# Kernel tuning notes

Hardware: AMD Instinct MI355X
Metric: run time of the kernel (lower is better)

Reference implementation:

```python
import jax, jax.numpy as jnp
import numpy as np

B, N, K = 8, 2048, 20
IN_CHAN = 3
CONV_DIMS = (64, 64, 128, 256)
FEAT_DIM = 1024
SLOPE = 0.2  # LeakyReLU negative slope (DGCNN standard)


def setup_inputs() -> dict:
    key = jax.random.key(0)
    ks = jax.random.split(key, 11)
    x = jax.random.normal(ks[0], (B, N, IN_CHAN), dtype=jnp.float32)
    in_dims = (IN_CHAN,) + CONV_DIMS[:-1]
    inp = {"x": x}
    for i, (cin, cout) in enumerate(zip(in_dims, CONV_DIMS)):
        inp[f"W{i+1}"] = jax.random.normal(ks[1 + 2 * i], (cout, 2 * cin), dtype=jnp.float32) * 0.05
        inp[f"b{i+1}"] = jnp.zeros((cout,), dtype=jnp.float32)
    inp["Wf"] = jax.random.normal(ks[9], (FEAT_DIM, sum(CONV_DIMS)), dtype=jnp.float32) * 0.05
    inp["bf"] = jnp.zeros((FEAT_DIM,), dtype=jnp.float32)
    return inp


def _knn_idx(x, k):
    # x: (B, N, C) -> indices of k nearest neighbors (self included), (B, N, K)
    xx = jnp.sum(x * x, axis=-1)                       # (B, N)
    inner = jnp.einsum('bnc,bmc->bnm', x, x)           # (B, N, N)
    d2 = xx[:, :, None] - 2.0 * inner + xx[:, None, :]  # squared distances
    _, idx = jax.lax.top_k(-d2, k)                     # k smallest distances
    return idx


def _edge_conv(x, W, b, k):
    # x: (B, N, C); W: (O, 2C); b: (O,) -> (B, N, O)
    idx = _knn_idx(x, k)                               # (B, N, K)
    nbr = jax.vmap(lambda xb, ib: xb[ib])(x, idx)      # (B, N, K, C) gather
    center = jnp.broadcast_to(x[:, :, None, :], nbr.shape)
    feat = jnp.concatenate([nbr - center, center], axis=-1)  # (B, N, K, 2C)
    h = jnp.einsum('bnkc,oc->bnko', feat, W) + b       # 1x1 conv over edges
    h = jax.nn.leaky_relu(h, SLOPE)
    return jnp.max(h, axis=2)                          # max over neighbors


def reference(x, W1, b1, W2, b2, W3, b3, W4, b4, Wf, bf):
    params = [(W1, b1), (W2, b2), (W3, b3), (W4, b4)]
    feats = []
    h = x
    for W, b in params:
        h = _edge_conv(h, W, b, K)
        feats.append(h)
    hcat = jnp.concatenate(feats, axis=-1)             # (B, N, sum(conv_dims))
    out = jnp.einsum('bnc,oc->bno', hcat, Wf) + bf     # final 1x1 conv
    out = jax.nn.leaky_relu(out, SLOPE)
    return jnp.max(out, axis=1)                        # global max pool -> (B, FEAT_DIM)
```

## Files before the change

kernel.cpp:

```cpp
#include <hip/hip_runtime.h>

constexpr int B_ = 8;
constexpr int N_ = 2048;
constexpr int K_ = 20;
constexpr float SLOPE_ = 0.2f;

typedef __attribute__((ext_vector_type(8))) short bf16x8;
typedef __attribute__((ext_vector_type(8))) _Float16 f16x8;
typedef __attribute__((ext_vector_type(4))) float f32x4;

__device__ __forceinline__ float lrelu(float v) { return v > 0.0f ? v : SLOPE_ * v; }

__device__ __forceinline__ void async16(const void* g, void* l) {
  __builtin_amdgcn_global_load_lds((const __attribute__((address_space(1))) unsigned int*)g,
                                   (__attribute__((address_space(3))) unsigned int*)l, 16, 0, 0);
}

__device__ __forceinline__ unsigned long long shflx64(unsigned long long v, int m) {
  return __shfl_xor(v, m, 64);
}

__device__ __forceinline__ unsigned short f2bf(float f) {
  unsigned u = __float_as_uint(f);
  u += 0x7fff + ((u >> 16) & 1);
  return (unsigned short)(u >> 16);
}

__device__ __forceinline__ unsigned short f2h(float f) {
  _Float16 h = (_Float16)f;
  return __builtin_bit_cast(unsigned short, h);
}
__device__ __forceinline__ float h2f(unsigned short u) {
  return (float)__builtin_bit_cast(_Float16, u);
}

__global__ void prep_wp(const float* __restrict__ W, float* __restrict__ Wp,
                        unsigned short* __restrict__ Wp_bf, int O, int C) {
  int i = blockIdx.x * 256 + threadIdx.x;
  if (i >= 2 * O * C) return;
  int o = i / C, c = i - o * C;
  float v;
  if (o < O)
    v = W[o * 2 * C + c];
  else
    v = W[(o - O) * 2 * C + C + c] - W[(o - O) * 2 * C + c];
  Wp[i] = v;
  if (Wp_bf) Wp_bf[i] = f2bf(v);
}

__global__ void cvt_bf16(const float4* __restrict__ src, ushort4* __restrict__ dst, int n4) {
  int i = blockIdx.x * 256 + threadIdx.x;
  if (i >= n4) return;
  float4 v = src[i];
  ushort4 o = {f2bf(v.x), f2bf(v.y), f2bf(v.z), f2bf(v.w)};
  dst[i] = o;
}

__global__ void split32_x(const float* __restrict__ x, unsigned short* __restrict__ xh,
                          unsigned short* __restrict__ xm, float* __restrict__ xx) {
  int id = blockIdx.x * 256 + threadIdx.x;
  if (id >= B_ * N_ * 32) return;
  int row = id >> 5, c = id & 31;
  float val = (c < 3) ? x[row * 3 + c] : 0.0f;
  unsigned short hb = f2h(val);
  float vh = h2f(hb);
  xh[id] = hb;
  xm[id] = f2h(val - vh);
  float sq = val * val;
#pragma unroll
  for (int off = 16; off > 0; off >>= 1) sq += __shfl_xor(sq, off, 32);
  if (c == 0) xx[row] = sq;
}

template <int C>
__global__ void pack_knn(const unsigned short* __restrict__ Xh,
                         const unsigned short* __restrict__ Xm,
                         unsigned short* __restrict__ Pk) {
  constexpr int KK = C / 32;
  int id = blockIdx.x * 256 + threadIdx.x;
  const int outoff = id;
  const int l = id & 63;
  id >>= 6;
  const int split = id & 1;
  id >>= 1;
  const int kk = id % KK;
  id /= KK;
  const int tile = id & 127;
  const int b = id >> 7;
  const unsigned short* src = (split == 0) ? Xh : Xm;
  const size_t soff =
      (size_t)(b * N_ + tile * 16 + (l & 15)) * C + (size_t)kk * 32 + (size_t)(l >> 4) * 8;
  uint4 v = *(const uint4*)(src + soff);
  *(uint4*)(Pk + (size_t)outoff * 8) = v;
}

__device__ __forceinline__ void select_topk(const float* __restrict__ d2row, int lane,
                                            unsigned long long* __restrict__ cb,
                                            int* __restrict__ outp) {
  float r2[32];
#pragma unroll
  for (int i = 0; i < 32; i++) r2[i] = d2row[i * 64 + lane];

  const float INF = __int_as_float(0x7f800000);

  float lmin = r2[0];
#pragma unroll
  for (int i = 1; i < 32; i++) lmin = fminf(lmin, r2[i]);
  float sv = lmin;
#pragma unroll
  for (int k = 2; k <= 64; k <<= 1)
#pragma unroll
    for (int j = k >> 1; j > 0; j >>= 1) {
      float p = __shfl_xor(sv, j, 64);
      bool takeMax = ((lane & j) != 0) == ((lane & k) == 0);
      sv = takeMax ? fmaxf(sv, p) : fminf(sv, p);
    }
  float T = __shfl(sv, 19, 64);

  unsigned cnt = 0;
#pragma unroll
  for (int i = 0; i < 32; i++) {
    bool pred = r2[i] <= T;
    unsigned long long mk = __ballot(pred);
    if (mk) {
      int off = __popcll(mk & ((1ull << lane) - 1ull));
      unsigned pos = cnt + (unsigned)off;
      if (pred && pos < 64)
        cb[pos] = ((unsigned long long)__float_as_uint(r2[i]) << 32) | (unsigned)(i * 64 + lane);
      cnt += (unsigned)__popcll(mk);
    }
  }

  if (cnt <= 64) {
    unsigned long long v = (lane < (int)cnt) ? cb[lane] : ~0ull;
#pragma unroll
    for (int k = 2; k <= 64; k <<= 1)
#pragma unroll
      for (int j = k >> 1; j > 0; j >>= 1) {
        unsigned long long p = shflx64(v, j);
        bool takeMax = ((lane & j) != 0) == ((lane & k) == 0);
        bool lt = v < p;
        v = (takeMax == lt) ? p : v;
      }
    if (lane < K_) outp[lane] = (int)(unsigned)(v & 0xffffffffull);
  } else {
    for (int t2 = 0; t2 < K_; t2++) {
      unsigned long long loc = ~0ull;
#pragma unroll
      for (int i = 0; i < 32; i++) {
        unsigned long long u =
            ((unsigned long long)__float_as_uint(r2[i]) << 32) | (unsigned)(i * 64 + lane);
        loc = u < loc ? u : loc;
      }
#pragma unroll
      for (int off = 32; off > 0; off >>= 1) {
        unsigned long long vv = shflx64(loc, off);
        loc = vv < loc ? vv : loc;
      }
      const int mwin = (int)(unsigned)(loc & 0xffffffffull);
      if (lane == 0) outp[t2] = mwin;
#pragma unroll
      for (int i = 0; i < 32; i++)
        if (i * 64 + lane == mwin) r2[i] = INF;
    }
  }
}

template <int C>
__global__ __launch_bounds__(1024, 4) void knn_mfma_q16(const unsigned short* __restrict__ Pk,
                                                        const unsigned short* __restrict__ Xh,
                                                        const unsigned short* __restrict__ Xm,
                                                        const float* __restrict__ xx,
                                                        int* __restrict__ idxo) {
  constexpr int KK = C / 32;
  constexpr int DP = 3;
  constexpr int NIT = KK * 8;
  const int b = blockIdx.x & 7;
  const int q0 = (blockIdx.x >> 3) * 16;
  const int tid = threadIdx.x;
  const int w = tid >> 6, lane = tid & 63;
  const int bN = b * N_;
  const int lr = lane & 15;
  const int lk = (lane >> 4) * 8;

  __shared__ float d2s[16][2052];
  __shared__ unsigned long long cbuf[16][64];

  const size_t qoff = (size_t)(bN + q0 + lr) * C + lk;
  f16x8 a2h[2], a2m[2];
  a2h[0] = *(const f16x8*)(Xh + qoff);
  a2m[0] = *(const f16x8*)(Xm + qoff);

  f32x4 acc[8];
#pragma unroll
  for (int t = 0; t < 8; t++) acc[t] = (f32x4){0.0f, 0.0f, 0.0f, 0.0f};

  const size_t pbase = (size_t)b * (128 * KK * 2 * 512) + (size_t)lane * 8;
  f16x8 bh[DP], bm[DP];
#pragma unroll
  for (int i = 0; i < DP; i++) {
    const size_t a = pbase + (size_t)(((w * 8 + i) * KK + 0) * 2) * 512;
    bh[i] = *(const f16x8*)(Pk + a);
    bm[i] = *(const f16x8*)(Pk + a + 512);
  }
#pragma unroll
  for (int it = 0; it < NIT; it++) {
    const int kk = it >> 3, t = it & 7, s = it % DP;
    if (t == 0 && kk + 1 < KK) {
      const size_t qa = qoff + (size_t)(kk + 1) * 32;
      a2h[(kk + 1) & 1] = *(const f16x8*)(Xh + qa);
      a2m[(kk + 1) & 1] = *(const f16x8*)(Xm + qa);
    }
    f16x8 vh = bh[s], vm = bm[s];
    if (it + DP < NIT) {
      const int it2 = it + DP;
      const int kk2 = it2 >> 3, t2 = it2 & 7;
      const size_t a = pbase + (size_t)(((w * 8 + t2) * KK + kk2) * 2) * 512;
      bh[s] = *(const f16x8*)(Pk + a);
      bm[s] = *(const f16x8*)(Pk + a + 512);
    }
    const f16x8 ah = a2h[kk & 1], am = a2m[kk & 1];
    acc[t] = __builtin_amdgcn_mfma_f32_16x16x32_f16(ah, vh, acc[t], 0, 0, 0);
    acc[t] = __builtin_amdgcn_mfma_f32_16x16x32_f16(ah, vm, acc[t], 0, 0, 0);
    acc[t] = __builtin_amdgcn_mfma_f32_16x16x32_f16(am, vh, acc[t], 0, 0, 0);
    acc[t] = __builtin_amdgcn_mfma_f32_16x16x32_f16(am, vm, acc[t], 0, 0, 0);
  }

  float qn[4];
#pragma unroll
  for (int r = 0; r < 4; r++) qn[r] = xx[bN + q0 + (lane >> 4) * 4 + r];
#pragma unroll
  for (int t = 0; t < 8; t++) {
    float cn = xx[bN + (w * 8 + t) * 16 + lr];
#pragma unroll
    for (int r = 0; r < 4; r++) {
      float v = fmaxf(fmaf(-2.0f, acc[t][r], cn + qn[r]), 0.0f);
      d2s[(lane >> 4) * 4 + r][(w * 8 + t) * 16 + lr] = v;
    }
  }
  __syncthreads();
  select_topk(&d2s[w][0], lane, cbuf[w], idxo + (size_t)(bN + q0 + w) * K_);
}

template <int C>
__global__ __launch_bounds__(512, 2) void knn_mfma_q32(const unsigned short* __restrict__ Pk,
                                                       const unsigned short* __restrict__ Xh,
                                                       const unsigned short* __restrict__ Xm,
                                                       const float* __restrict__ xx,
                                                       int* __restrict__ idxo) {
  constexpr int KK = C / 32;
  constexpr int NIT = KK * 16;
  const int b = blockIdx.x & 7;
  const int q0 = (blockIdx.x >> 3) * 32;
  const int tid = threadIdx.x;
  const int w = tid >> 6, lane = tid & 63;
  const int bN = b * N_;
  const int lr = lane & 15;
  const int lk = (lane >> 4) * 8;

  __shared__ float d2s[16][2052];
  __shared__ unsigned long long cbuf[8][64];

  const size_t qoff0 = (size_t)(bN + q0 + lr) * C + lk;
  const size_t qoff1 = (size_t)(bN + q0 + 16 + lr) * C + lk;

  f32x4 acc0[16], acc1[16];
#pragma unroll
  for (int t = 0; t < 16; t++) {
    acc0[t] = (f32x4){0.0f, 0.0f, 0.0f, 0.0f};
    acc1[t] = (f32x4){0.0f, 0.0f, 0.0f, 0.0f};
  }

  const size_t pbase = (size_t)b * (128 * KK * 2 * 512) + (size_t)lane * 8;
  f16x8 bh[2], bm[2];
#pragma unroll
  for (int i = 0; i < 2; i++) {
    const size_t a = pbase + (size_t)(((w * 16 + i) * KK + 0) * 2) * 512;
    bh[i] = *(const f16x8*)(Pk + a);
    bm[i] = *(const f16x8*)(Pk + a + 512);
  }
  f16x8 ah0, am0, ah1, am1;
#pragma unroll
  for (int it = 0; it < NIT; it++) {
    const int kk = it >> 4, t = it & 15, s = it & 1;
    if (t == 0) {
      ah0 = *(const f16x8*)(Xh + qoff0 + (size_t)kk * 32);
      am0 = *(const f16x8*)(Xm + qoff0 + (size_t)kk * 32);
      ah1 = *(const f16x8*)(Xh + qoff1 + (size_t)kk * 32);
      am1 = *(const f16x8*)(Xm + qoff1 + (size_t)kk * 32);
    }
    f16x8 vh = bh[s], vm = bm[s];
    if (it + 2 < NIT) {
      const int it2 = it + 2;
      const int kk2 = it2 >> 4, t2 = it2 & 15;
      const size_t a = pbase + (size_t)(((w * 16 + t2) * KK + kk2) * 2) * 512;
      bh[s] = *(const f16x8*)(Pk + a);
      bm[s] = *(const f16x8*)(Pk + a + 512);
    }
    acc0[t] = __builtin_amdgcn_mfma_f32_16x16x32_f16(ah0, vh, acc0[t], 0, 0, 0);
    acc0[t] = __builtin_amdgcn_mfma_f32_16x16x32_f16(ah0, vm, acc0[t], 0, 0, 0);
    acc0[t] = __builtin_amdgcn_mfma_f32_16x16x32_f16(am0, vh, acc0[t], 0, 0, 0);
    acc0[t] = __builtin_amdgcn_mfma_f32_16x16x32_f16(am0, vm, acc0[t], 0, 0, 0);
    acc1[t] = __builtin_amdgcn_mfma_f32_16x16x32_f16(ah1, vh, acc1[t], 0, 0, 0);
    acc1[t] = __builtin_amdgcn_mfma_f32_16x16x32_f16(ah1, vm, acc1[t], 0, 0, 0);
    acc1[t] = __builtin_amdgcn_mfma_f32_16x16x32_f16(am1, vh, acc1[t], 0, 0, 0);
    acc1[t] = __builtin_amdgcn_mfma_f32_16x16x32_f16(am1, vm, acc1[t], 0, 0, 0);
  }

  float qn0[4], qn1[4];
#pragma unroll
  for (int r = 0; r < 4; r++) {
    qn0[r] = xx[bN + q0 + (lane >> 4) * 4 + r];
    qn1[r] = xx[bN + q0 + 16 + (lane >> 4) * 4 + r];
  }

#pragma unroll
  for (int t = 0; t < 16; t++) {
    const int tt = w * 16 + t;
    float cn = xx[bN + tt * 16 + lr];
#pragma unroll
    for (int r = 0; r < 4; r++)
      d2s[(lane >> 4) * 4 + r][tt * 16 + lr] = fmaxf(fmaf(-2.0f, acc0[t][r], cn + qn0[r]), 0.0f);
  }
  __syncthreads();
  select_topk(&d2s[2 * w + 0][0], lane, cbuf[w], idxo + (size_t)(bN + q0 + 2 * w + 0) * K_);
  select_topk(&d2s[2 * w + 1][0], lane, cbuf[w], idxo + (size_t)(bN + q0 + 2 * w + 1) * K_);
  __syncthreads();

#pragma unroll
  for (int t = 0; t < 16; t++) {
    const int tt = w * 16 + t;
    float cn = xx[bN + tt * 16 + lr];
#pragma unroll
    for (int r = 0; r < 4; r++)
      d2s[(lane >> 4) * 4 + r][tt * 16 + lr] = fmaxf(fmaf(-2.0f, acc1[t][r], cn + qn1[r]), 0.0f);
  }
  __syncthreads();
  select_topk(&d2s[2 * w + 0][0], lane, cbuf[w], idxo + (size_t)(bN + q0 + 16 + 2 * w + 0) * K_);
  select_topk(&d2s[2 * w + 1][0], lane, cbuf[w], idxo + (size_t)(bN + q0 + 16 + 2 * w + 1) * K_);
}

template <int C, int O2>
__global__ void proj_kernel(const float* __restrict__ hin, int stride,
                            const float* __restrict__ Wp, float* __restrict__ P) {
  const int nt = (blockIdx.x & 7) * N_ + (blockIdx.x >> 3) * 16;
  const int o = blockIdx.y * blockDim.x + threadIdx.x;
  __shared__ float hs[16][C];
  for (int i = threadIdx.x; i < 16 * C; i += blockDim.x) {
    int r = i / C, c = i - r * C;
    hs[r][c] = hin[(size_t)(nt + r) * stride + c];
  }
  __syncthreads();
  float acc[16];
#pragma unroll
  for (int t = 0; t < 16; t++) acc[t] = 0.0f;
  const float* wr = Wp + (size_t)o * C;
  if constexpr (C % 4 == 0) {
    for (int cg = 0; cg < C; cg += 4) {
      float4 w = *(const float4*)(wr + cg);
#pragma unroll
      for (int t = 0; t < 16; t++) {
        float4 h = *(const float4*)(&hs[t][cg]);
        acc[t] += w.x * h.x + w.y * h.y + w.z * h.z + w.w * h.w;
      }
    }
  } else {
    for (int c = 0; c < C; c++) {
      float w = wr[c];
#pragma unroll
      for (int t = 0; t < 16; t++) acc[t] += w * hs[t][c];
    }
  }
#pragma unroll
  for (int t = 0; t < 16; t++) P[(size_t)(nt + t) * O2 + o] = acc[t];
}

__global__ __launch_bounds__(256) void gemm_proj(const unsigned short* __restrict__ A, int astride,
                                                 const unsigned short* __restrict__ Bw,
                                                 float* __restrict__ P) {
  const int m0 = ((blockIdx.x & 7) * 16 + (blockIdx.x >> 3)) * 128;
  const int n0 = blockIdx.y * 128;
  const int tid = threadIdx.x;
  const int w = tid >> 6, lane = tid & 63;
  const int wm = w & 1, wn = w >> 1;

  __shared__ unsigned short lA[128 * 32];
  __shared__ unsigned short lB[128 * 32];

  const int r0 = (w * 2 + 0) * 16 + (lane >> 2);
  const int r1 = (w * 2 + 1) * 16 + (lane >> 2);
  const int ks = (lane & 3) * 8;
  const unsigned short* a0 = A + (size_t)(m0 + r0) * astride + ks;
  const unsigned short* a1 = A + (size_t)(m0 + r1) * astride + ks;
  const unsigned short* b0 = Bw + (size_t)(n0 + r0) * 128 + ks;
  const unsigned short* b1 = Bw + (size_t)(n0 + r1) * 128 + ks;
  unsigned short* lA0 = lA + (w * 2 + 0) * 512;
  unsigned short* lA1 = lA + (w * 2 + 1) * 512;
  unsigned short* lB0 = lB + (w * 2 + 0) * 512;
  unsigned short* lB1 = lB + (w * 2 + 1) * 512;

  f32x4 acc[4][4] = {};
  const int ka = (lane >> 4) * 8;

  for (int k0 = 0; k0 < 128; k0 += 32) {
    __syncthreads();
    async16(a0 + k0, lA0);
    async16(a1 + k0, lA1);
    async16(b0 + k0, lB0);
    async16(b1 + k0, lB1);
    __syncthreads();
    bf16x8 af[4], bfr[4];
#pragma unroll
    for (int mt = 0; mt < 4; mt++)
      af[mt] = *(const bf16x8*)&lA[(wm * 64 + mt * 16 + (lane & 15)) * 32 + ka];
#pragma unroll
    for (int nt = 0; nt < 4; nt++)
      bfr[nt] = *(const bf16x8*)&lB[(wn * 64 + nt * 16 + (lane & 15)) * 32 + ka];
#pragma unroll
    for (int mt = 0; mt < 4; mt++)
#pragma unroll
      for (int nt = 0; nt < 4; nt++)
        acc[mt][nt] = __builtin_amdgcn_mfma_f32_16x16x32_bf16(af[mt], bfr[nt], acc[mt][nt], 0, 0, 0);
  }

  const int col = n0 + wn * 64 + (lane & 15);
  const int rowb = m0 + wm * 64 + (lane >> 4) * 4;
#pragma unroll
  for (int mt = 0; mt < 4; mt++)
#pragma unroll
    for (int nt = 0; nt < 4; nt++)
#pragma unroll
      for (int r = 0; r < 4; r++)
        P[(size_t)(rowb + mt * 16 + r) * 512 + col + nt * 16] = acc[mt][nt][r];
}

template <int O>
__global__ __launch_bounds__(256) void combine_kernel(
    const float* __restrict__ P, const int* __restrict__ idxo, const float* __restrict__ bias,
    float* __restrict__ hout, unsigned short* __restrict__ hbf, float* __restrict__ xxo,
    unsigned short* __restrict__ xh, unsigned short* __restrict__ xm,
    unsigned short* __restrict__ a4) {
  constexpr int ROWS = 256 / O;
  const int bb = blockIdx.x & 7;
  const int rt = blockIdx.x >> 3;
  const int r = threadIdx.x / O;
  const int o = threadIdx.x & (O - 1);
  const int row = bb * N_ + rt * ROWS + r;
  __shared__ int idxs[ROWS][K_];
  __shared__ float ps[ROWS][O / 64 > 0 ? O / 64 : 1];
  if (o < K_) idxs[r][o] = idxo[(size_t)row * K_ + o];
  __syncthreads();
  const int base_row = bb * N_;
  float g = -3.4e38f;
#pragma unroll
  for (int k = 0; k < K_; k++) {
    float v = P[(size_t)(base_row + idxs[r][k]) * (2 * O) + o];
    g = fmaxf(g, v);
  }
  float ba = P[(size_t)row * (2 * O) + O + o];
  float val = lrelu(g + ba + bias[o]);
  if (hout) hout[(size_t)row * 512 + o] = val;
  if (hbf) hbf[(size_t)row * 512 + o] = f2bf(val);
  if (xh) {
    unsigned short hb = f2h(val);
    float vh = h2f(hb);
    size_t pp = (size_t)row * O + o;
    xh[pp] = hb;
    xm[pp] = f2h(val - vh);
  }
  if (a4) a4[(size_t)row * 1024 + o] = f2bf(val);
  if (xxo) {
    float sq = val * val;
#pragma unroll
    for (int off = 32; off > 0; off >>= 1) sq += __shfl_xor(sq, off, 64);
    if constexpr (O == 64) {
      if (o == 0) xxo[row] = sq;
    } else {
      if ((threadIdx.x & 63) == 0) ps[r][o >> 6] = sq;
      __syncthreads();
      if (o == 0) {
        float t = ps[r][0];
#pragma unroll
        for (int u = 1; u < O / 64; u++) t += ps[r][u];
        xxo[row] = t;
      }
    }
  }
}

__global__ __launch_bounds__(256) void gemm_final(const unsigned short* __restrict__ A,
                                                  const unsigned short* __restrict__ Bw,
                                                  float* __restrict__ part) {
  const int mt5 = (blockIdx.x & 7) * 16 + (blockIdx.x >> 3);
  const int m0 = mt5 * 128;
  const int n0 = blockIdx.y * 128;
  const int tid = threadIdx.x;
  const int w = tid >> 6, lane = tid & 63;
  const int wm = w & 1, wn = w >> 1;

  __shared__ unsigned short lA[128 * 32];
  __shared__ unsigned short lB[128 * 32];
  __shared__ float ldsred[2][128];

  const int r0 = (w * 2 + 0) * 16 + (lane >> 2);
  const int r1 = (w * 2 + 1) * 16 + (lane >> 2);
  const int ks = (lane & 3) * 8;
  const unsigned short* a0 = A + (size_t)(m0 + r0) * 512 + ks;
  const unsigned short* a1 = A + (size_t)(m0 + r1) * 512 + ks;
  const unsigned short* b0 = Bw + (size_t)(n0 + r0) * 512 + ks;
  const unsigned short* b1 = Bw + (size_t)(n0 + r1) * 512 + ks;
  unsigned short* lA0 = lA + (w * 2 + 0) * 512;
  unsigned short* lA1 = lA + (w * 2 + 1) * 512;
  unsigned short* lB0 = lB + (w * 2 + 0) * 512;
  unsigned short* lB1 = lB + (w * 2 + 1) * 512;

  f32x4 acc[4][4] = {};
  const int ka = (lane >> 4) * 8;

  for (int k0 = 0; k0 < 512; k0 += 32) {
    __syncthreads();
    async16(a0 + k0, lA0);
    async16(a1 + k0, lA1);
    async16(b0 + k0, lB0);
    async16(b1 + k0, lB1);
    __syncthreads();
    bf16x8 af[4], bfr[4];
#pragma unroll
    for (int mt = 0; mt < 4; mt++)
      af[mt] = *(const bf16x8*)&lA[(wm * 64 + mt * 16 + (lane & 15)) * 32 + ka];
#pragma unroll
    for (int nt = 0; nt < 4; nt++)
      bfr[nt] = *(const bf16x8*)&lB[(wn * 64 + nt * 16 + (lane & 15)) * 32 + ka];
#pragma unroll
    for (int mt = 0; mt < 4; mt++)
#pragma unroll
      for (int nt = 0; nt < 4; nt++)
        acc[mt][nt] = __builtin_amdgcn_mfma_f32_16x16x32_bf16(af[mt], bfr[nt], acc[mt][nt], 0, 0, 0);
  }

#pragma unroll
  for (int nt = 0; nt < 4; nt++) {
    float v = -3.4e38f;
#pragma unroll
    for (int mt = 0; mt < 4; mt++)
#pragma unroll
      for (int r = 0; r < 4; r++) v = fmaxf(v, acc[mt][nt][r]);
    v = fmaxf(v, __shfl_xor(v, 16, 64));
    v = fmaxf(v, __shfl_xor(v, 32, 64));
    if (lane < 16) ldsred[wm][wn * 64 + nt * 16 + lane] = v;
  }
  __syncthreads();
  if (tid < 128) {
    float v = fmaxf(ldsred[0][tid], ldsred[1][tid]);
    const int b = blockIdx.x & 7, s5 = blockIdx.x >> 3;
    part[(size_t)(b * 16 + s5) * 1024 + n0 + tid] = v;
  }
}

__global__ void final_reduce(const float* __restrict__ part, const float* __restrict__ bf,
                             float* __restrict__ out) {
  int i = blockIdx.x * 256 + threadIdx.x;
  if (i >= B_ * 1024) return;
  int b = i >> 10, o = i & 1023;
  float m = -3.4e38f;
  for (int s = 0; s < 16; s++) m = fmaxf(m, part[(size_t)(b * 16 + s) * 1024 + o]);
  out[i] = lrelu(m + bf[o]);
}

extern "C" void kernel_launch(void* const* d_in, const int* in_sizes, int n_in, void* d_out,
                              int out_size, void* d_ws, size_t ws_size, hipStream_t stream) {
  (void)in_sizes; (void)n_in; (void)out_size;
  const float* x = (const float*)d_in[0];
  const float* W1 = (const float*)d_in[1];
  const float* b1 = (const float*)d_in[2];
  const float* W2 = (const float*)d_in[3];
  const float* b2 = (const float*)d_in[4];
  const float* W3 = (const float*)d_in[5];
  const float* b3 = (const float*)d_in[6];
  const float* W4 = (const float*)d_in[7];
  const float* b4 = (const float*)d_in[8];
  const float* Wf = (const float*)d_in[9];
  const float* bf = (const float*)d_in[10];

  float* ws = (float*)d_ws;
  float* hcat = ws;
  float* P = hcat + (size_t)B_ * N_ * 512;
  int* idx = (int*)(P + (size_t)B_ * N_ * 512);
  float* Wp = (float*)(idx + (size_t)B_ * N_ * K_);
  float* part = Wp + 512 * 128;
  float* xxb = part + 8 * 16 * 1024;
  float* out = (float*)d_out;
  unsigned short* hcat_bf = (unsigned short*)P;
  unsigned short* Wf_bf = hcat_bf + (size_t)B_ * N_ * 512;
  unsigned short* A4_bf = (unsigned short*)hcat + 512;
  unsigned short* Wp_bf = (unsigned short*)part;

  float* ws_end = xxb + (size_t)B_ * N_;
  unsigned short* hcatbf2 = (unsigned short*)ws_end;
  const size_t need = ((char*)(hcatbf2 + (size_t)B_ * N_ * 512)) - (char*)d_ws;
  const bool fused = ws_size >= need;

  unsigned short* Xh23 = (unsigned short*)(P + (size_t)2097152);
  unsigned short* Xm23 = Xh23 + (size_t)B_ * N_ * 64;
  unsigned short* Xh4 = (unsigned short*)(P + (size_t)4194304);
  unsigned short* Xm4 = Xh4 + (size_t)B_ * N_ * 128;
  unsigned short* Xh1 = Xh23;
  unsigned short* Xm1 = Xh1 + (size_t)B_ * N_ * 32;
  unsigned short* Pk = (unsigned short*)P;

  dim3 knng16(N_ / 16 * B_);
  dim3 knng32q(N_ / 32 * B_);
  const int pk_blocks32 = B_ * 128 * 1 * 2 * 64 / 256;
  const int pk_blocks64 = B_ * 128 * 2 * 2 * 64 / 256;
  const int pk_blocks128 = B_ * 128 * 4 * 2 * 64 / 256;

  prep_wp<<<(2 * 64 * 3 + 255) / 256, 256, 0, stream>>>(W1, Wp, nullptr, 64, 3);
  split32_x<<<(B_ * N_ * 32 + 255) / 256, 256, 0, stream>>>(x, Xh1, Xm1, xxb);
  pack_knn<32><<<pk_blocks32, 256, 0, stream>>>(Xh1, Xm1, Pk);
  knn_mfma_q16<32><<<knng16, 1024, 0, stream>>>(Pk, Xh1, Xm1, xxb, idx);
  proj_kernel<3, 128><<<dim3(B_ * N_ / 16, 1), 128, 0, stream>>>(x, 3, Wp, P);
  combine_kernel<64><<<B_ * N_ / 4, 256, 0, stream>>>(
      P, idx, b1, hcat + 0, fused ? hcatbf2 + 0 : nullptr, xxb, Xh23, Xm23, nullptr);

  prep_wp<<<(2 * 64 * 64 + 255) / 256, 256, 0, stream>>>(W2, Wp, nullptr, 64, 64);
  pack_knn<64><<<pk_blocks64, 256, 0, stream>>>(Xh23, Xm23, Pk);
  knn_mfma_q16<64><<<knng16, 1024, 0, stream>>>(Pk, Xh23, Xm23, xxb, idx);
  proj_kernel<64, 128><<<dim3(B_ * N_ / 16, 1), 128, 0, stream>>>(hcat + 0, 512, Wp, P);
  combine_kernel<64><<<B_ * N_ / 4, 256, 0, stream>>>(
      P, idx, b2, hcat + 64, fused ? hcatbf2 + 64 : nullptr, xxb, Xh23, Xm23, nullptr);

  prep_wp<<<(2 * 128 * 64 + 255) / 256, 256, 0, stream>>>(W3, Wp, nullptr, 128, 64);
  pack_knn<64><<<pk_blocks64, 256, 0, stream>>>(Xh23, Xm23, Pk);
  knn_mfma_q32<64><<<knng32q, 512, 0, stream>>>(Pk, Xh23, Xm23, xxb, idx);
  proj_kernel<64, 256><<<dim3(B_ * N_ / 16, 1), 256, 0, stream>>>(hcat + 64, 512, Wp, P);
  combine_kernel<128><<<B_ * N_ / 2, 256, 0, stream>>>(
      P, idx, b3, fused ? nullptr : hcat + 128, fused ? hcatbf2 + 128 : nullptr, xxb, Xh4, Xm4,
      A4_bf);

  prep_wp<<<(2 * 256 * 128 + 255) / 256, 256, 0, stream>>>(W4, Wp, Wp_bf, 256, 128);
  pack_knn<128><<<pk_blocks128, 256, 0, stream>>>(Xh4, Xm4, Pk);
  knn_mfma_q32<128><<<knng32q, 512, 0, stream>>>(Pk, Xh4, Xm4, xxb, idx);
  gemm_proj<<<dim3(B_ * N_ / 128, 4), 256, 0, stream>>>(A4_bf, 1024, Wp_bf, P);
  combine_kernel<256><<<B_ * N_, 256, 0, stream>>>(
      P, idx, b4, fused ? nullptr : hcat + 256, fused ? hcatbf2 + 256 : nullptr, nullptr,
      nullptr, nullptr, nullptr);

  if (!fused)
    cvt_bf16<<<(B_ * N_ * 512 / 4 + 255) / 256, 256, 0, stream>>>(
        (const float4*)hcat, (ushort4*)hcat_bf, B_ * N_ * 512 / 4);
  cvt_bf16<<<(1024 * 512 / 4 + 255) / 256, 256, 0, stream>>>(
      (const float4*)Wf, (ushort4*)Wf_bf, 1024 * 512 / 4);
  gemm_final<<<dim3(128, 8), 256, 0, stream>>>(fused ? hcatbf2 : hcat_bf, Wf_bf, part);
  final_reduce<<<(B_ * 1024 + 255) / 256, 256, 0, stream>>>(part, bf, out);
}
```

Before: 439.5 us.

## Write kNN features directly in MFMA-packed layout and drop pack_knn kernels

The producer kernels (split32_x and combine_kernel) now write the fp16 hi/lo split features straight into the tiled, lane-interleaved layout the MFMA kNN kernels consume. This removes the separate pack_knn passes. The kNN kernels read their query fragments from the same packed buffer instead of row-major Xh/Xm arrays. Layer 2 also switches from the q16 kNN kernel to the q32 variant. Stores in the producers become scattered 2-byte writes, which may coalesce less well.

```diff
diff --git a/kernel.cpp b/kernel.cpp
--- a/kernel.cpp
+++ b/kernel.cpp
@@ -33,6 +33,7 @@
 __device__ __forceinline__ float h2f(unsigned short u) {
   return (float)__builtin_bit_cast(_Float16, u);
 }
+
 
 __global__ void prep_wp(const float* __restrict__ W, float* __restrict__ Wp,
                         unsigned short* __restrict__ Wp_bf, int O, int C) {
@@ -56,42 +57,25 @@
   dst[i] = o;
 }
 
-__global__ void split32_x(const float* __restrict__ x, unsigned short* __restrict__ xh,
-                          unsigned short* __restrict__ xm, float* __restrict__ xx) {
+__global__ void split32_x(const float* __restrict__ x, unsigned short* __restrict__ Pk1,
+                          float* __restrict__ xx) {
   int id = blockIdx.x * 256 + threadIdx.x;
   if (id >= B_ * N_ * 32) return;
   int row = id >> 5, c = id & 31;
   float val = (c < 3) ? x[row * 3 + c] : 0.0f;
   unsigned short hb = f2h(val);
   float vh = h2f(hb);
-  xh[id] = hb;
-  xm[id] = f2h(val - vh);
+  unsigned short mb = f2h(val - vh);
+  const int b = row >> 11, n = row & (N_ - 1);
+  const int tile = n >> 4, rr = n & 15;
+  const int lane = ((c >> 3) << 4) + rr, elem = c & 7;
+  const size_t chunk = (size_t)(b * 128 + tile) * 2 * 512;
+  Pk1[chunk + lane * 8 + elem] = hb;
+  Pk1[chunk + 512 + lane * 8 + elem] = mb;
   float sq = val * val;
 #pragma unroll
   for (int off = 16; off > 0; off >>= 1) sq += __shfl_xor(sq, off, 32);
   if (c == 0) xx[row] = sq;
-}
-
-template <int C>
-__global__ void pack_knn(const unsigned short* __restrict__ Xh,
-                         const unsigned short* __restrict__ Xm,
-                         unsigned short* __restrict__ Pk) {
-  constexpr int KK = C / 32;
-  int id = blockIdx.x * 256 + threadIdx.x;
-  const int outoff = id;
-  const int l = id & 63;
-  id >>= 6;
-  const int split = id & 1;
-  id >>= 1;
-  const int kk = id % KK;
-  id /= KK;
-  const int tile = id & 127;
-  const int b = id >> 7;
-  const unsigned short* src = (split == 0) ? Xh : Xm;
-  const size_t soff =
-      (size_t)(b * N_ + tile * 16 + (l & 15)) * C + (size_t)kk * 32 + (size_t)(l >> 4) * 8;
-  uint4 v = *(const uint4*)(src + soff);
-  *(uint4*)(Pk + (size_t)outoff * 8) = v;
 }
 
 __device__ __forceinline__ void select_topk(const float* __restrict__ d2row, int lane,
@@ -168,8 +152,6 @@
 
 template <int C>
 __global__ __launch_bounds__(1024, 4) void knn_mfma_q16(const unsigned short* __restrict__ Pk,
-                                                        const unsigned short* __restrict__ Xh,
-                                                        const unsigned short* __restrict__ Xm,
                                                         const float* __restrict__ xx,
                                                         int* __restrict__ idxo) {
   constexpr int KK = C / 32;
@@ -181,15 +163,14 @@
   const int w = tid >> 6, lane = tid & 63;
   const int bN = b * N_;
   const int lr = lane & 15;
-  const int lk = (lane >> 4) * 8;
 
   __shared__ float d2s[16][2052];
   __shared__ unsigned long long cbuf[16][64];
 
-  const size_t qoff = (size_t)(bN + q0 + lr) * C + lk;
+  const size_t qchunk = (size_t)(b * 128 + (q0 >> 4)) * KK * 2 * 512 + (size_t)lane * 8;
   f16x8 a2h[2], a2m[2];
-  a2h[0] = *(const f16x8*)(Xh + qoff);
-  a2m[0] = *(const f16x8*)(Xm + qoff);
+  a2h[0] = *(const f16x8*)(Pk + qchunk);
+  a2m[0] = *(const f16x8*)(Pk + qchunk + 512);
 
   f32x4 acc[8];
 #pragma unroll
@@ -207,9 +188,9 @@
   for (int it = 0; it < NIT; it++) {
     const int kk = it >> 3, t = it & 7, s = it % DP;
     if (t == 0 && kk + 1 < KK) {
-      const size_t qa = qoff + (size_t)(kk + 1) * 32;
-      a2h[(kk + 1) & 1] = *(const f16x8*)(Xh + qa);
-      a2m[(kk + 1) & 1] = *(const f16x8*)(Xm + qa);
+      const size_t qa = qchunk + (size_t)(kk + 1) * 2 * 512;
+      a2h[(kk + 1) & 1] = *(const f16x8*)(Pk + qa);
+      a2m[(kk + 1) & 1] = *(const f16x8*)(Pk + qa + 512);
     }
     f16x8 vh = bh[s], vm = bm[s];
     if (it + DP < NIT) {
@@ -244,8 +225,6 @@
 
 template <int C>
 __global__ __launch_bounds__(512, 2) void knn_mfma_q32(const unsigned short* __restrict__ Pk,
-                                                       const unsigned short* __restrict__ Xh,
-                                                       const unsigned short* __restrict__ Xm,
                                                        const float* __restrict__ xx,
                                                        int* __restrict__ idxo) {
   constexpr int KK = C / 32;
@@ -256,13 +235,12 @@
   const int w = tid >> 6, lane = tid & 63;
   const int bN = b * N_;
   const int lr = lane & 15;
-  const int lk = (lane >> 4) * 8;
 
   __shared__ float d2s[16][2052];
   __shared__ unsigned long long cbuf[8][64];
 
-  const size_t qoff0 = (size_t)(bN + q0 + lr) * C + lk;
-  const size_t qoff1 = (size_t)(bN + q0 + 16 + lr) * C + lk;
+  const size_t qc0 = (size_t)(b * 128 + (q0 >> 4)) * KK * 2 * 512 + (size_t)lane * 8;
+  const size_t qc1 = (size_t)(b * 128 + (q0 >> 4) + 1) * KK * 2 * 512 + (size_t)lane * 8;
 
   f32x4 acc0[16], acc1[16];
 #pragma unroll
@@ -284,10 +262,12 @@
   for (int it = 0; it < NIT; it++) {
     const int kk = it >> 4, t = it & 15, s = it & 1;
     if (t == 0) {
-      ah0 = *(const f16x8*)(Xh + qoff0 + (size_t)kk * 32);
-      am0 = *(const f16x8*)(Xm + qoff0 + (size_t)kk * 32);
-      ah1 = *(const f16x8*)(Xh + qoff1 + (size_t)kk * 32);
-      am1 = *(const f16x8*)(Xm + qoff1 + (size_t)kk * 32);
+      const size_t a0 = qc0 + (size_t)kk * 2 * 512;
+      const size_t a1 = qc1 + (size_t)kk * 2 * 512;
+      ah0 = *(const f16x8*)(Pk + a0);
+      am0 = *(const f16x8*)(Pk + a0 + 512);
+      ah1 = *(const f16x8*)(Pk + a1);
+      am1 = *(const f16x8*)(Pk + a1 + 512);
     }
     f16x8 vh = bh[s], vm = bm[s];
     if (it + 2 < NIT) {
@@ -438,8 +418,7 @@
 __global__ __launch_bounds__(256) void combine_kernel(
     const float* __restrict__ P, const int* __restrict__ idxo, const float* __restrict__ bias,
     float* __restrict__ hout, unsigned short* __restrict__ hbf, float* __restrict__ xxo,
-    unsigned short* __restrict__ xh, unsigned short* __restrict__ xm,
-    unsigned short* __restrict__ a4) {
+    unsigned short* __restrict__ pk, unsigned short* __restrict__ a4) {
   constexpr int ROWS = 256 / O;
   const int bb = blockIdx.x & 7;
   const int rt = blockIdx.x >> 3;
@@ -461,12 +440,17 @@
   float val = lrelu(g + ba + bias[o]);
   if (hout) hout[(size_t)row * 512 + o] = val;
   if (hbf) hbf[(size_t)row * 512 + o] = f2bf(val);
-  if (xh) {
+  if (pk) {
     unsigned short hb = f2h(val);
     float vh = h2f(hb);
-    size_t pp = (size_t)row * O + o;
-    xh[pp] = hb;
-    xm[pp] = f2h(val - vh);
+    unsigned short mb = f2h(val - vh);
+    const int n = rt * ROWS + r;
+    const int tile = n >> 4, rr = n & 15;
+    const int kk = o >> 5, cc = o & 31;
+    const int lane2 = ((cc >> 3) << 4) + rr, elem = cc & 7;
+    const size_t chunk = ((size_t)(bb * 128 + tile) * (O / 32) + kk) * 2 * 512;
+    pk[chunk + lane2 * 8 + elem] = hb;
+    pk[chunk + 512 + lane2 * 8 + elem] = mb;
   }
   if (a4) a4[(size_t)row * 1024 + o] = f2bf(val);
   if (xxo) {
@@ -600,50 +584,38 @@
   const size_t need = ((char*)(hcatbf2 + (size_t)B_ * N_ * 512)) - (char*)d_ws;
   const bool fused = ws_size >= need;
 
-  unsigned short* Xh23 = (unsigned short*)(P + (size_t)2097152);
-  unsigned short* Xm23 = Xh23 + (size_t)B_ * N_ * 64;
-  unsigned short* Xh4 = (unsigned short*)(P + (size_t)4194304);
-  unsigned short* Xm4 = Xh4 + (size_t)B_ * N_ * 128;
-  unsigned short* Xh1 = Xh23;
-  unsigned short* Xm1 = Xh1 + (size_t)B_ * N_ * 32;
-  unsigned short* Pk = (unsigned short*)P;
+  unsigned short* Pk23 = (unsigned short*)(P + (size_t)2097152);
+  unsigned short* Pk4 = (unsigned short*)(P + (size_t)4194304);
 
   dim3 knng16(N_ / 16 * B_);
   dim3 knng32q(N_ / 32 * B_);
-  const int pk_blocks32 = B_ * 128 * 1 * 2 * 64 / 256;
-  const int pk_blocks64 = B_ * 128 * 2 * 2 * 64 / 256;
-  const int pk_blocks128 = B_ * 128 * 4 * 2 * 64 / 256;
 
   prep_wp<<<(2 * 64 * 3 + 255) / 256, 256, 0, stream>>>(W1, Wp, nullptr, 64, 3);
-  split32_x<<<(B_ * N_ * 32 + 255) / 256, 256, 0, stream>>>(x, Xh1, Xm1, xxb);
-  pack_knn<32><<<pk_blocks32, 256, 0, stream>>>(Xh1, Xm1, Pk);
-  knn_mfma_q16<32><<<knng16, 1024, 0, stream>>>(Pk, Xh1, Xm1, xxb, idx);
+  split32_x<<<(B_ * N_ * 32 + 255) / 256, 256, 0, stream>>>(x, Pk23, xxb);
+  knn_mfma_q16<32><<<knng16, 1024, 0, stream>>>(Pk23, xxb, idx);
   proj_kernel<3, 128><<<dim3(B_ * N_ / 16, 1), 128, 0, stream>>>(x, 3, Wp, P);
   combine_kernel<64><<<B_ * N_ / 4, 256, 0, stream>>>(
-      P, idx, b1, hcat + 0, fused ? hcatbf2 + 0 : nullptr, xxb, Xh23, Xm23, nullptr);
+      P, idx, b1, hcat + 0, fused ? hcatbf2 + 0 : nullptr, xxb, Pk23, nullptr);
 
   prep_wp<<<(2 * 64 * 64 + 255) / 256, 256, 0, stream>>>(W2, Wp, nullptr, 64, 64);
-  pack_knn<64><<<pk_blocks64, 256, 0, stream>>>(Xh23, Xm23, Pk);
-  knn_mfma_q16<64><<<knng16, 1024, 0, stream>>>(Pk, Xh23, Xm23, xxb, idx);
+  knn_mfma_q32<64><<<knng32q, 512, 0, stream>>>(Pk23, xxb, idx);
   proj_kernel<64, 128><<<dim3(B_ * N_ / 16, 1), 128, 0, stream>>>(hcat + 0, 512, Wp, P);
   combine_kernel<64><<<B_ * N_ / 4, 256, 0, stream>>>(
-      P, idx, b2, hcat + 64, fused ? hcatbf2 + 64 : nullptr, xxb, Xh23, Xm23, nullptr);
+      P, idx, b2, hcat + 64, fused ? hcatbf2 + 64 : nullptr, xxb, Pk23, nullptr);
 
   prep_wp<<<(2 * 128 * 64 + 255) / 256, 256, 0, stream>>>(W3, Wp, nullptr, 128, 64);
-  pack_knn<64><<<pk_blocks64, 256, 0, stream>>>(Xh23, Xm23, Pk);
-  knn_mfma_q32<64><<<knng32q, 512, 0, stream>>>(Pk, Xh23, Xm23, xxb, idx);
+  knn_mfma_q32<64><<<knng32q, 512, 0, stream>>>(Pk23, xxb, idx);
   proj_kernel<64, 256><<<dim3(B_ * N_ / 16, 1), 256, 0, stream>>>(hcat + 64, 512, Wp, P);
   combine_kernel<128><<<B_ * N_ / 2, 256, 0, stream>>>(
-      P, idx, b3, fused ? nullptr : hcat + 128, fused ? hcatbf2 + 128 : nullptr, xxb, Xh4, Xm4,
+      P, idx, b3, fused ? nullptr : hcat + 128, fused ? hcatbf2 + 128 : nullptr, xxb, Pk4,
       A4_bf);
 
   prep_wp<<<(2 * 256 * 128 + 255) / 256, 256, 0, stream>>>(W4, Wp, Wp_bf, 256, 128);
-  pack_knn<128><<<pk_blocks128, 256, 0, stream>>>(Xh4, Xm4, Pk);
-  knn_mfma_q32<128><<<knng32q, 512, 0, stream>>>(Pk, Xh4, Xm4, xxb, idx);
+  knn_mfma_q32<128><<<knng32q, 512, 0, stream>>>(Pk4, xxb, idx);
   gemm_proj<<<dim3(B_ * N_ / 128, 4), 256, 0, stream>>>(A4_bf, 1024, Wp_bf, P);
   combine_kernel<256><<<B_ * N_, 256, 0, stream>>>(
       P, idx, b4, fused ? nullptr : hcat + 256, fused ? hcatbf2 + 256 : nullptr, nullptr,
-      nullptr, nullptr, nullptr);
+      nullptr, nullptr);
 
   if (!fused)
     cvt_bf16<<<(B_ * N_ * 512 / 4 + 255) / 256, 256, 0, stream>>>(
```

Result: faster. 408.1 us, median of 2 (-7.1%).
